# Kernel optimization log

Measured on AMD Instinct MI355X. Metric: run time of the kernel, lower is better.

The kernel has to match this reference:

```python
import jax, jax.numpy as jnp
import numpy as np

GRID_RES = 128
GRID_MIN, GRID_MAX = -1.0, 1.0
SIGMA = 0.1
EPS = 1e-5


def _make_grid_points():
    coords = jnp.linspace(GRID_MIN, GRID_MAX, GRID_RES)
    grid_y, grid_x = jnp.meshgrid(coords, coords, indexing='ij')
    # (2, M) with M = GRID_RES**2; channel 0 = x, channel 1 = y (matches torch buffer)
    return jnp.stack([grid_x, grid_y], axis=0).reshape(2, -1).astype(jnp.float32)


def setup_inputs() -> dict:
    key = jax.random.key(0)
    k1, k2 = jax.random.split(key)
    B, N = 4, 4096
    x_c = jax.random.uniform(k1, (B, N, 2), dtype=jnp.float32)   # in grid_range
    y_c = jax.random.uniform(k2, (B, N, 1), dtype=jnp.float32)
    grid_points = _make_grid_points()                            # (2, M)
    mask = jnp.ones((B, N), dtype=bool)
    return {"x_c": x_c, "y_c": y_c, "grid_points": grid_points, "mask": mask}


def reference(x_c, y_c, grid_points, mask):
    # x_c: (B,N,2), y_c: (B,N,1), grid_points: (2,M), mask: (B,N) bool
    B = x_c.shape[0]
    # pairwise squared distances: (B,N,2,M) diff -> (B,N,M)
    diff = x_c[:, :, :, None] - grid_points[None, None, :, :]
    dists_sq = jnp.sum(diff * diff, axis=2)
    weights = jnp.exp(-0.5 * dists_sq / (SIGMA * SIGMA))        # (B,N,M)
    weights = weights * mask[:, :, None].astype(weights.dtype)
    density = jnp.sum(weights, axis=1)                           # (B,M)
    # bmm: (B,1,N) @ (B,N,M) -> (B,1,M)
    weighted_sum = jnp.einsum('bnf,bnm->bfm', y_c, weights)[:, 0]  # (B,M)
    normalized = weighted_sum / (density + EPS)
    out = jnp.stack([density, normalized], axis=1)               # (B,2,M)
    return out.reshape(B, 2, GRID_RES, GRID_RES)
```

## Files before the change

kernel.cpp:

```cpp
#include <hip/hip_runtime.h>
#include <hip/hip_bf16.h>
#include <math.h>

#define GRID_RES 128
#define M_TOT (GRID_RES * GRID_RES)
#define N_PTS 4096
#define B_SZ 4
#define KS 16
#define GT 4
#define SLAB 32
#define KC 256
#define KP 264
#define NEG50_LOG2E -72.134752044448170f

typedef __attribute__((ext_vector_type(8))) short short8;
typedef __attribute__((ext_vector_type(4))) float f32x4;

static __device__ __forceinline__ unsigned short f2bf(float f) {
    __hip_bfloat16 h = __float2bfloat16(f);
    unsigned short u;
    __builtin_memcpy(&u, &h, 2);
    return u;
}
static __device__ __forceinline__ unsigned int pack_bf16(float a, float b) {
    return (unsigned int)f2bf(a) | ((unsigned int)f2bf(b) << 16);
}
static __device__ __forceinline__ float bf2f(unsigned short u) {
    unsigned int v = ((unsigned int)u) << 16;
    float f;
    __builtin_memcpy(&f, &v, 4);
    return f;
}

__global__ __launch_bounds__(512) void mfma_gemm(const float* __restrict__ x_c,
                                                 const float* __restrict__ y_c,
                                                 const int* __restrict__ mask,
                                                 const float* __restrict__ gp,
                                                 unsigned short* __restrict__ partial) {
    const int ks = blockIdx.x;
    const int gt = blockIdx.y;
    const int b  = blockIdx.z;
    const int t  = threadIdx.x;
    const int n0 = ks * KC;
    const int gy0 = gt * SLAB;
    const size_t inoff = (size_t)b * N_PTS;

    __shared__ __align__(16) unsigned short Wy_lds[SLAB][KP];
    __shared__ __align__(16) unsigned short Yw_lds[SLAB][KP];
    __shared__ __align__(16) unsigned short Wx_lds[128][KP];
    __shared__ float pxs[KC], pys[KC], s0s[KC], s1s[KC];
    __shared__ float cxs[128], cys[SLAB];

    if (t < KC) {
        const float2 xy = *(const float2*)&x_c[(inoff + n0 + t) * 2];
        pxs[t] = xy.x;
        pys[t] = xy.y;
        const float mk = (mask[inoff + n0 + t] != 0) ? 1.0f : 0.0f;
        s0s[t] = mk;
        s1s[t] = mk * y_c[inoff + n0 + t];
    } else if (t < 384) {
        cxs[t - 256] = gp[t - 256];
    } else if (t < 384 + SLAB) {
        cys[t - 384] = gp[M_TOT + (gy0 + t - 384) * GRID_RES];
    }
    __syncthreads();

    {
        const int k2 = t & 127;
        const int r0 = t >> 7;
        const float px0 = pxs[2 * k2], px1 = pxs[2 * k2 + 1];
        const float py0 = pys[2 * k2], py1 = pys[2 * k2 + 1];
        const float m0  = s0s[2 * k2], m1  = s0s[2 * k2 + 1];
        const float v0  = s1s[2 * k2], v1  = s1s[2 * k2 + 1];
        #pragma unroll 4
        for (int j = 0; j < 32; ++j) {
            const int r = r0 + 4 * j;
            const float cb = cxs[r];
            const float d0 = px0 - cb, d1 = px1 - cb;
            *(unsigned int*)&Wx_lds[r][2 * k2] =
                pack_bf16(exp2f(NEG50_LOG2E * d0 * d0), exp2f(NEG50_LOG2E * d1 * d1));
        }
        #pragma unroll 2
        for (int j = 0; j < 8; ++j) {
            const int r = r0 + 4 * j;
            const float ca = cys[r];
            const float d0 = py0 - ca, d1 = py1 - ca;
            const float w0 = exp2f(NEG50_LOG2E * d0 * d0);
            const float w1 = exp2f(NEG50_LOG2E * d1 * d1);
            *(unsigned int*)&Wy_lds[r][2 * k2] = pack_bf16(w0 * m0, w1 * m1);
            *(unsigned int*)&Yw_lds[r][2 * k2] = pack_bf16(w0 * v0, w1 * v1);
        }
    }
    __syncthreads();

    const int w  = t >> 6;
    const int l  = t & 63;
    const int lr = l & 15;
    const int lg = l >> 4;
    const int ch = w >> 2;
    const int c0 = (w & 3) * 32;
    const unsigned short (*A)[KP] = ch ? Yw_lds : Wy_lds;

    f32x4 acc[2][2];
    #pragma unroll
    for (int rf = 0; rf < 2; ++rf)
        #pragma unroll
        for (int cf = 0; cf < 2; ++cf)
            acc[rf][cf] = (f32x4){0.f, 0.f, 0.f, 0.f};

    #pragma unroll
    for (int s = 0; s < 8; ++s) {
        const int koff = s * 32 + lg * 8;
        const short8 a0 = *(const short8*)&A[lr][koff];
        const short8 a1 = *(const short8*)&A[16 + lr][koff];
        const short8 b0 = *(const short8*)&Wx_lds[c0 + lr][koff];
        const short8 b1 = *(const short8*)&Wx_lds[c0 + 16 + lr][koff];
        acc[0][0] = __builtin_amdgcn_mfma_f32_16x16x32_bf16(a0, b0, acc[0][0], 0, 0, 0);
        acc[0][1] = __builtin_amdgcn_mfma_f32_16x16x32_bf16(a0, b1, acc[0][1], 0, 0, 0);
        acc[1][0] = __builtin_amdgcn_mfma_f32_16x16x32_bf16(a1, b0, acc[1][0], 0, 0, 0);
        acc[1][1] = __builtin_amdgcn_mfma_f32_16x16x32_bf16(a1, b1, acc[1][1], 0, 0, 0);
    }

    unsigned short* pt = partial + ((((size_t)ks * B_SZ + b) * 2 + ch) << 14);
    #pragma unroll
    for (int rf = 0; rf < 2; ++rf)
        #pragma unroll
        for (int cf = 0; cf < 2; ++cf)
            #pragma unroll
            for (int r = 0; r < 4; ++r) {
                const int row = gy0 + rf * 16 + lg * 4 + r;
                const int col = c0 + cf * 16 + lr;
                pt[row * GRID_RES + col] = f2bf(acc[rf][cf][r]);
            }
}

__global__ __launch_bounds__(256) void reduce_kernel(const unsigned short* __restrict__ partial,
                                                     float* __restrict__ out) {
    const int idx = blockIdx.x * 256 + threadIdx.x;
    const int b  = idx >> 11;
    const int m0 = (idx & 2047) * 8;
    float d[8], v[8];
    #pragma unroll
    for (int j = 0; j < 8; ++j) { d[j] = 0.f; v[j] = 0.f; }
    for (int ks = 0; ks < KS; ++ks) {
        const short8 pd = *(const short8*)&partial[((((size_t)ks * B_SZ + b) * 2 + 0) << 14) + m0];
        const short8 pv = *(const short8*)&partial[((((size_t)ks * B_SZ + b) * 2 + 1) << 14) + m0];
        #pragma unroll
        for (int j = 0; j < 8; ++j) {
            d[j] += bf2f((unsigned short)pd[j]);
            v[j] += bf2f((unsigned short)pv[j]);
        }
    }
    float* od = out + (((size_t)b * 2 + 0) << 14) + m0;
    float* ov = out + (((size_t)b * 2 + 1) << 14) + m0;
    *(float4*)&od[0] = make_float4(d[0], d[1], d[2], d[3]);
    *(float4*)&od[4] = make_float4(d[4], d[5], d[6], d[7]);
    *(float4*)&ov[0] = make_float4(v[0] / (d[0] + 1e-5f), v[1] / (d[1] + 1e-5f),
                                   v[2] / (d[2] + 1e-5f), v[3] / (d[3] + 1e-5f));
    *(float4*)&ov[4] = make_float4(v[4] / (d[4] + 1e-5f), v[5] / (d[5] + 1e-5f),
                                   v[6] / (d[6] + 1e-5f), v[7] / (d[7] + 1e-5f));
}

extern "C" void kernel_launch(void* const* d_in, const int* in_sizes, int n_in,
                              void* d_out, int out_size, void* d_ws, size_t ws_size,
                              hipStream_t stream) {
    const float* x_c  = (const float*)d_in[0];
    const float* y_c  = (const float*)d_in[1];
    const float* gp   = (const float*)d_in[2];
    const int* mask   = (const int*)d_in[3];
    float* out = (float*)d_out;

    unsigned short* partial = (unsigned short*)d_ws;

    mfma_gemm<<<dim3(KS, GT, B_SZ), 512, 0, stream>>>(x_c, y_c, mask, gp, partial);
    reduce_kernel<<<(B_SZ * M_TOT / 8) / 256, 256, 0, stream>>>(partial, out);
}
```

Baseline: 16.88 us.

## Fuse GEMM and reduction into one cooperative kernel with grid sync

Merges the MFMA partial-GEMM kernel and the split-K reduction kernel into a single cooperative launch, separated by a grid-wide barrier. The aim is to remove the second kernel launch and the inter-kernel gap. In exchange, the reduction now runs on 256 blocks of 512 threads with scalar bf16 loads instead of 8-wide vector loads. It also adds the cost of a cooperative grid sync and requires the whole grid to be co-resident.

```diff
diff --git a/kernel.cpp b/kernel.cpp
--- a/kernel.cpp
+++ b/kernel.cpp
@@ -1,6 +1,9 @@
 #include <hip/hip_runtime.h>
+#include <hip/hip_cooperative_groups.h>
 #include <hip/hip_bf16.h>
 #include <math.h>
+
+namespace cg = cooperative_groups;
 
 #define GRID_RES 128
 #define M_TOT (GRID_RES * GRID_RES)
@@ -32,11 +35,12 @@
     return f;
 }
 
-__global__ __launch_bounds__(512) void mfma_gemm(const float* __restrict__ x_c,
+__global__ __launch_bounds__(512) void fused_all(const float* __restrict__ x_c,
                                                  const float* __restrict__ y_c,
                                                  const int* __restrict__ mask,
                                                  const float* __restrict__ gp,
-                                                 unsigned short* __restrict__ partial) {
+                                                 unsigned short* __restrict__ partial,
+                                                 float* __restrict__ out) {
     const int ks = blockIdx.x;
     const int gt = blockIdx.y;
     const int b  = blockIdx.z;
@@ -93,72 +97,64 @@
     }
     __syncthreads();
 
-    const int w  = t >> 6;
-    const int l  = t & 63;
-    const int lr = l & 15;
-    const int lg = l >> 4;
-    const int ch = w >> 2;
-    const int c0 = (w & 3) * 32;
-    const unsigned short (*A)[KP] = ch ? Yw_lds : Wy_lds;
+    {
+        const int w  = t >> 6;
+        const int l  = t & 63;
+        const int lr = l & 15;
+        const int lg = l >> 4;
+        const int ch = w >> 2;
+        const int c0 = (w & 3) * 32;
+        const unsigned short (*A)[KP] = ch ? Yw_lds : Wy_lds;
 
-    f32x4 acc[2][2];
-    #pragma unroll
-    for (int rf = 0; rf < 2; ++rf)
+        f32x4 acc[2][2];
         #pragma unroll
-        for (int cf = 0; cf < 2; ++cf)
-            acc[rf][cf] = (f32x4){0.f, 0.f, 0.f, 0.f};
+        for (int rf = 0; rf < 2; ++rf)
+            #pragma unroll
+            for (int cf = 0; cf < 2; ++cf)
+                acc[rf][cf] = (f32x4){0.f, 0.f, 0.f, 0.f};
 
-    #pragma unroll
-    for (int s = 0; s < 8; ++s) {
-        const int koff = s * 32 + lg * 8;
-        const short8 a0 = *(const short8*)&A[lr][koff];
-        const short8 a1 = *(const short8*)&A[16 + lr][koff];
-        const short8 b0 = *(const short8*)&Wx_lds[c0 + lr][koff];
-        const short8 b1 = *(const short8*)&Wx_lds[c0 + 16 + lr][koff];
-        acc[0][0] = __builtin_amdgcn_mfma_f32_16x16x32_bf16(a0, b0, acc[0][0], 0, 0, 0);
-        acc[0][1] = __builtin_amdgcn_mfma_f32_16x16x32_bf16(a0, b1, acc[0][1], 0, 0, 0);
-        acc[1][0] = __builtin_amdgcn_mfma_f32_16x16x32_bf16(a1, b0, acc[1][0], 0, 0, 0);
-        acc[1][1] = __builtin_amdgcn_mfma_f32_16x16x32_bf16(a1, b1, acc[1][1], 0, 0, 0);
+        #pragma unroll
+        for (int s = 0; s < 8; ++s) {
+            const int koff = s * 32 + lg * 8;
+            const short8 a0 = *(const short8*)&A[lr][koff];
+            const short8 a1 = *(const short8*)&A[16 + lr][koff];
+            const short8 b0 = *(const short8*)&Wx_lds[c0 + lr][koff];
+            const short8 b1 = *(const short8*)&Wx_lds[c0 + 16 + lr][koff];
+            acc[0][0] = __builtin_amdgcn_mfma_f32_16x16x32_bf16(a0, b0, acc[0][0], 0, 0, 0);
+            acc[0][1] = __builtin_amdgcn_mfma_f32_16x16x32_bf16(a0, b1, acc[0][1], 0, 0, 0);
+            acc[1][0] = __builtin_amdgcn_mfma_f32_16x16x32_bf16(a1, b0, acc[1][0], 0, 0, 0);
+            acc[1][1] = __builtin_amdgcn_mfma_f32_16x16x32_bf16(a1, b1, acc[1][1], 0, 0, 0);
+        }
+
+        unsigned short* pt = partial + ((((size_t)ks * B_SZ + b) * 2 + ch) << 14);
+        #pragma unroll
+        for (int rf = 0; rf < 2; ++rf)
+            #pragma unroll
+            for (int cf = 0; cf < 2; ++cf)
+                #pragma unroll
+                for (int r = 0; r < 4; ++r) {
+                    const int row = gy0 + rf * 16 + lg * 4 + r;
+                    const int col = c0 + cf * 16 + lr;
+                    pt[row * GRID_RES + col] = f2bf(acc[rf][cf][r]);
+                }
     }
 
-    unsigned short* pt = partial + ((((size_t)ks * B_SZ + b) * 2 + ch) << 14);
-    #pragma unroll
-    for (int rf = 0; rf < 2; ++rf)
-        #pragma unroll
-        for (int cf = 0; cf < 2; ++cf)
-            #pragma unroll
-            for (int r = 0; r < 4; ++r) {
-                const int row = gy0 + rf * 16 + lg * 4 + r;
-                const int col = c0 + cf * 16 + lr;
-                pt[row * GRID_RES + col] = f2bf(acc[rf][cf][r]);
-            }
-}
+    cg::this_grid().sync();
 
-__global__ __launch_bounds__(256) void reduce_kernel(const unsigned short* __restrict__ partial,
-                                                     float* __restrict__ out) {
-    const int idx = blockIdx.x * 256 + threadIdx.x;
-    const int b  = idx >> 11;
-    const int m0 = (idx & 2047) * 8;
-    float d[8], v[8];
-    #pragma unroll
-    for (int j = 0; j < 8; ++j) { d[j] = 0.f; v[j] = 0.f; }
-    for (int ks = 0; ks < KS; ++ks) {
-        const short8 pd = *(const short8*)&partial[((((size_t)ks * B_SZ + b) * 2 + 0) << 14) + m0];
-        const short8 pv = *(const short8*)&partial[((((size_t)ks * B_SZ + b) * 2 + 1) << 14) + m0];
-        #pragma unroll
-        for (int j = 0; j < 8; ++j) {
-            d[j] += bf2f((unsigned short)pd[j]);
-            v[j] += bf2f((unsigned short)pv[j]);
+    const int flat = blockIdx.x + KS * (blockIdx.y + GT * blockIdx.z);
+    const int gidx = flat * 512 + t;
+    if (gidx < B_SZ * M_TOT) {
+        const int b2 = gidx >> 14;
+        const int m  = gidx & (M_TOT - 1);
+        float dsum = 0.f, vsum = 0.f;
+        #pragma unroll 4
+        for (int k2 = 0; k2 < KS; ++k2) {
+            dsum += bf2f(partial[((((size_t)k2 * B_SZ + b2) * 2 + 0) << 14) + m]);
+            vsum += bf2f(partial[((((size_t)k2 * B_SZ + b2) * 2 + 1) << 14) + m]);
         }
+        out[(((size_t)b2 * 2 + 0) << 14) + m] = dsum;
+        out[(((size_t)b2 * 2 + 1) << 14) + m] = vsum / (dsum + 1e-5f);
     }
-    float* od = out + (((size_t)b * 2 + 0) << 14) + m0;
-    float* ov = out + (((size_t)b * 2 + 1) << 14) + m0;
-    *(float4*)&od[0] = make_float4(d[0], d[1], d[2], d[3]);
-    *(float4*)&od[4] = make_float4(d[4], d[5], d[6], d[7]);
-    *(float4*)&ov[0] = make_float4(v[0] / (d[0] + 1e-5f), v[1] / (d[1] + 1e-5f),
-                                   v[2] / (d[2] + 1e-5f), v[3] / (d[3] + 1e-5f));
-    *(float4*)&ov[4] = make_float4(v[4] / (d[4] + 1e-5f), v[5] / (d[5] + 1e-5f),
-                                   v[6] / (d[6] + 1e-5f), v[7] / (d[7] + 1e-5f));
 }
 
 extern "C" void kernel_launch(void* const* d_in, const int* in_sizes, int n_in,
@@ -172,6 +168,8 @@
 
     unsigned short* partial = (unsigned short*)d_ws;
 
-    mfma_gemm<<<dim3(KS, GT, B_SZ), 512, 0, stream>>>(x_c, y_c, mask, gp, partial);
-    reduce_kernel<<<(B_SZ * M_TOT / 8) / 256, 256, 0, stream>>>(partial, out);
+    void* args[] = {(void*)&x_c, (void*)&y_c, (void*)&mask, (void*)&gp,
+                    (void*)&partial, (void*)&out};
+    hipLaunchCooperativeKernel((const void*)fused_all, dim3(KS, GT, B_SZ), dim3(512),
+                               args, 0, stream);
 }
```

Result: slower. 58.11 us (+244.2%).
